# Performance work log

Measured on AMD Instinct MI355X. Metric: run time of the kernel, lower is better.

## Reference

```python
import jax, jax.numpy as jnp
import numpy as np

K_TOP = 2  # n_experts_per_tok
W_SCALE = 0.02  # keep activations numerically tame


def setup_inputs() -> dict:
    key = jax.random.key(0)
    ks = jax.random.split(key, 8)
    D, F, E = 1024, 1024, 8
    B, T = 4, 2048
    x = jax.random.normal(ks[0], (B, T, D), dtype=jnp.float32)
    router_w = jax.random.normal(ks[1], (D, E), dtype=jnp.float32) * W_SCALE
    sg = jax.random.normal(ks[2], (D, F), dtype=jnp.float32) * W_SCALE
    su = jax.random.normal(ks[3], (D, F), dtype=jnp.float32) * W_SCALE
    sd = jax.random.normal(ks[4], (F, D), dtype=jnp.float32) * W_SCALE
    wg = jax.random.normal(ks[5], (E, D, F), dtype=jnp.float32) * W_SCALE
    wu = jax.random.normal(ks[6], (E, D, F), dtype=jnp.float32) * W_SCALE
    wd = jax.random.normal(ks[7], (E, F, D), dtype=jnp.float32) * W_SCALE
    return {"x": x, "router_w": router_w, "sg": sg, "su": su, "sd": sd,
            "wg": wg, "wu": wu, "wd": wd}


def reference(x, router_w, sg, su, sd, wg, wu, wd):
    B, T, D = x.shape
    E = wg.shape[0]
    flat = x.reshape(-1, D)                       # [N, D]
    N = flat.shape[0]

    # shared SwiGLU expert (n_shared_experts = 1)
    shared = (jax.nn.silu(flat @ sg) * (flat @ su)) @ sd  # [N, D]

    # top-k softmax router with renormalization
    probs = jax.nn.softmax(flat @ router_w, axis=-1)      # [N, E]
    topk_p, topk_i = jax.lax.top_k(probs, K_TOP)          # [N, K]
    topk_p = topk_p / (jnp.sum(topk_p, axis=-1, keepdims=True) + 1e-9)

    # dense combine weights: scatter renormalized probs into [N, E]
    cw = jnp.zeros((N, E), dtype=flat.dtype).at[
        jnp.arange(N)[:, None], topk_i].add(topk_p)

    # per-expert SwiGLU on all tokens, weighted combine (jit-friendly MoE form)
    h = jax.nn.silu(jnp.einsum('nd,edf->nef', flat, wg)) \
        * jnp.einsum('nd,edf->nef', flat, wu)             # [N, E, F]
    eo = jnp.einsum('nef,efd->ned', h, wd)                # [N, E, D]
    routed = jnp.einsum('ned,ne->nd', eo, cw)             # [N, D]

    return (shared + routed).reshape(B, T, D)
```

## Files before the change

kernel.cpp:

```cpp
#include <hip/hip_runtime.h>

#define N_TOK    8192
#define D_DIM    1024
#define F_DIM    1024
#define NESH     9
#define MAX_RTD  17408
#define MAX_ROWS 26624
#define BT 128
#define BK 32
#define NK 32

#define MO 16
#define MT 25

typedef float  f4    __attribute__((ext_vector_type(4)));
typedef float  f32x4 __attribute__((ext_vector_type(4)));
typedef short  s16x8 __attribute__((ext_vector_type(8)));
typedef unsigned short u16x8 __attribute__((ext_vector_type(8)));
typedef unsigned short u16x4 __attribute__((ext_vector_type(4)));

static __device__ __forceinline__ unsigned short f2bf(float f) {
    union { float f; unsigned u; } v; v.f = f;
    unsigned r = v.u + 0x7FFFu + ((v.u >> 16) & 1u);
    return (unsigned short)(r >> 16);
}
static __device__ __forceinline__ float bf2f(unsigned short u) {
    union { unsigned u; float f; } v; v.u = ((unsigned)u) << 16; return v.f;
}

#define GLDS(gp, lp) __builtin_amdgcn_global_load_lds( \
    (const __attribute__((address_space(1))) void*)(gp), \
    (__attribute__((address_space(3))) void*)(lp), 16, 0, 0)

__global__ __launch_bounds__(256) void k_transpose(
    const float* __restrict__ wg, const float* __restrict__ wu,
    const float* __restrict__ wd, const float* __restrict__ sg,
    const float* __restrict__ su, const float* __restrict__ sd,
    unsigned short* __restrict__ wgt, unsigned short* __restrict__ wut,
    unsigned short* __restrict__ wdt)
{
    int bx = blockIdx.x;
    int m = bx >> 8;
    int tile = bx & 255;
    int ty = tile >> 4, tx = tile & 15;
    int set = m / 9, e = m % 9;
    const float* src; unsigned short* dst;
    if (set == 0)      { src = (e < 8) ? wg + (size_t)e*1048576 : sg; dst = wgt + (size_t)e*1048576; }
    else if (set == 1) { src = (e < 8) ? wu + (size_t)e*1048576 : su; dst = wut + (size_t)e*1048576; }
    else               { src = (e < 8) ? wd + (size_t)e*1048576 : sd; dst = wdt + (size_t)e*1048576; }

    __shared__ unsigned short ts[64 * 67];
    int t = threadIdx.x;
    int rT0 = ty * 64, cT0 = tx * 64;
    #pragma unroll
    for (int i = 0; i < 4; i++) {
        int idx = t + i * 256;
        int a  = idx >> 4;
        int b4 = (idx & 15) * 4;
        f4 v = *(const f4*)(src + (size_t)(cT0 + a) * 1024 + rT0 + b4);
        ts[a * 67 + b4 + 0] = f2bf(v[0]);
        ts[a * 67 + b4 + 1] = f2bf(v[1]);
        ts[a * 67 + b4 + 2] = f2bf(v[2]);
        ts[a * 67 + b4 + 3] = f2bf(v[3]);
    }
    __syncthreads();
    #pragma unroll
    for (int i = 0; i < 2; i++) {
        int slot = t + i * 256;
        int r  = slot >> 3;
        int c8 = (slot & 7) * 8;
        u16x8 o;
        #pragma unroll
        for (int k = 0; k < 8; k++) o[k] = ts[(c8 + k) * 67 + r];
        *(u16x8*)&dst[(size_t)(rT0 + r) * 1024 + cT0 + c8] = o;
    }
}

__global__ __launch_bounds__(256) void k_router(
    const float* __restrict__ x, const float* __restrict__ rw,
    unsigned short* __restrict__ xb,
    int* __restrict__ tk_i, float* __restrict__ tk_w)
{
    int wid = threadIdx.x >> 6, lane = threadIdx.x & 63;
    int n = blockIdx.x * 4 + wid;
    const float* xr = x + (size_t)n * D_DIM;
    unsigned short* xbr = xb + (size_t)n * D_DIM;
    float acc[8] = {0,0,0,0,0,0,0,0};
    #pragma unroll
    for (int it = 0; it < 4; it++) {
        int d0 = it * 256 + lane * 4;
        f4 xv = *(const f4*)(xr + d0);
        #pragma unroll
        for (int j = 0; j < 4; j++) {
            f4 r0 = *(const f4*)(rw + (size_t)(d0 + j) * 8);
            f4 r1 = *(const f4*)(rw + (size_t)(d0 + j) * 8 + 4);
            acc[0] += xv[j]*r0[0]; acc[1] += xv[j]*r0[1]; acc[2] += xv[j]*r0[2]; acc[3] += xv[j]*r0[3];
            acc[4] += xv[j]*r1[0]; acc[5] += xv[j]*r1[1]; acc[6] += xv[j]*r1[2]; acc[7] += xv[j]*r1[3];
        }
        u16x4 o; o[0]=f2bf(xv[0]); o[1]=f2bf(xv[1]); o[2]=f2bf(xv[2]); o[3]=f2bf(xv[3]);
        *(u16x4*)&xbr[d0] = o;
    }
    #pragma unroll
    for (int e = 0; e < 8; e++)
        for (int off = 32; off; off >>= 1)
            acc[e] += __shfl_xor(acc[e], off, 64);
    if (lane == 0) {
        float mx = acc[0];
        for (int e = 1; e < 8; e++) mx = fmaxf(mx, acc[e]);
        float p[8], s = 0.f;
        for (int e = 0; e < 8; e++) { p[e] = expf(acc[e] - mx); s += p[e]; }
        int i0 = 0;
        for (int e = 1; e < 8; e++) if (p[e] > p[i0]) i0 = e;
        int i1 = (i0 == 0) ? 1 : 0;
        for (int e = 0; e < 8; e++) if (e != i0 && p[e] > p[i1]) i1 = e;
        float p0 = p[i0] / s, p1 = p[i1] / s;
        float rs = p0 + p1 + 1e-9f;
        tk_i[2*n] = i0;  tk_i[2*n+1] = i1;
        tk_w[2*n] = p0 / rs;  tk_w[2*n+1] = p1 / rs;
    }
}

__global__ __launch_bounds__(1024) void k_count_scatter(
    const int* __restrict__ tk_i, const float* __restrict__ tk_w,
    int* __restrict__ meta,
    int* __restrict__ row_token, int* __restrict__ row_expert,
    int* __restrict__ tok_pos)
{
    __shared__ int cnt[1024 * 9];
    __shared__ int tot[8];
    __shared__ int off[9];
    const int t = threadIdx.x;
    const int lane = t & 63;
    const int wid = t >> 6;

    #pragma unroll
    for (int e = 0; e < 8; e++) cnt[t * 9 + e] = 0;
    __syncthreads();

    #pragma unroll
    for (int j = 0; j < 8; j++) {
        int n = t * 8 + j;
        cnt[t * 9 + tk_i[2 * n]]++;
        cnt[t * 9 + tk_i[2 * n + 1]]++;
    }
    __syncthreads();

    if (wid < 8) {
        const int e = wid;
        int carry = 0;
        for (int c = 0; c < 16; c++) {
            int i = c * 64 + lane;
            int v = cnt[i * 9 + e];
            int s = v;
            #pragma unroll
            for (int d = 1; d < 64; d <<= 1) {
                int u = __shfl_up(s, d, 64);
                if (lane >= d) s += u;
            }
            cnt[i * 9 + e] = s - v + carry;
            carry += __shfl(s, 63, 64);
        }
        if (lane == 0) tot[e] = carry;
    }
    __syncthreads();

    if (t == 0) {
        int acc = 0;
        #pragma unroll
        for (int e = 0; e < 8; e++) {
            off[e] = acc;
            meta[MO + e] = acc;
            acc += ((tot[e] + 127) >> 7) << 7;
        }
        off[8] = acc;
        meta[MO + 8] = acc;
        meta[MT] = acc + N_TOK;
    }
    __syncthreads();

    #pragma unroll
    for (int j = 0; j < 8; j++) {
        int n = t * 8 + j;
        #pragma unroll
        for (int k = 0; k < 2; k++) {
            int e = tk_i[2 * n + k];
            int pos = off[e] + cnt[t * 9 + e];
            cnt[t * 9 + e] = cnt[t * 9 + e] + 1;
            row_token[pos] = n; row_expert[pos] = e;
            tok_pos[2 * n + k] = pos;
        }
        int ps = off[8] + n;
        row_token[ps] = n; row_expert[ps] = 8;
    }
    #pragma unroll
    for (int e = 0; e < 8; e++) {
        int start = off[e] + tot[e], end = off[e + 1];
        for (int i = start + t; i < end; i += 1024) row_token[i] = -1;
    }
}


__global__ __launch_bounds__(512, 4) void k_gemm1(
    const unsigned short* __restrict__ xb,
    const unsigned short* __restrict__ wgt,
    const unsigned short* __restrict__ wut,
    const int* __restrict__ row_token,
    const int* __restrict__ row_expert,
    const int* __restrict__ meta,
    unsigned short* __restrict__ h)
{
    const int total = meta[MT];
    const int orig = blockIdx.x;
    const int bid = (orig & 7) * 208 + (orig >> 3);
    const int rt = bid >> 3, ct = bid & 7;
    const int row0 = rt * BT;
    if (row0 >= total) return;
    const int e = row_expert[row0];

    __shared__ __align__(16) unsigned short sA[2 * 128 * 32];
    __shared__ __align__(16) unsigned short sBg[2 * 128 * 32];
    __shared__ __align__(16) unsigned short sBu[2 * 128 * 32];

    const int t = threadIdx.x;
    const int lane = t & 63;
    const int lr = lane & 15;
    const int kl = lane >> 4;
    const int wid = t >> 6;
    const int wr = wid >> 2, wc = wid & 3;

    const int srow = t >> 2;
    const int scg  = (t & 3) ^ ((srow >> 1) & 3);
    int tok = row_token[row0 + srow];
    if (tok < 0) tok = 0;
    const unsigned short* srcA = xb + (size_t)tok * D_DIM + scg * 8;
    const unsigned short* srcG = wgt + ((size_t)e * F_DIM + ct * BT + srow) * D_DIM + scg * 8;
    const unsigned short* srcU = wut + ((size_t)e * F_DIM + ct * BT + srow) * D_DIM + scg * 8;

    f32x4 accg[4][2] = {}, accu[4][2] = {};

#define ST1(bb, k0) do { \
    GLDS(srcA + (k0), &sA[(bb) * 4096 + t * 8]); \
    GLDS(srcG + (k0), &sBg[(bb) * 4096 + t * 8]); \
    GLDS(srcU + (k0), &sBu[(bb) * 4096 + t * 8]); } while (0)

#define COMPUTE1(bb) do { \
    const unsigned short* pA  = &sA[(bb) * 4096]; \
    const unsigned short* pG  = &sBg[(bb) * 4096]; \
    const unsigned short* pU  = &sBu[(bb) * 4096]; \
    s16x8 a_[4], g_[2], q_[2]; \
    _Pragma("unroll") \
    for (int m_ = 0; m_ < 4; m_++) { \
        int row = wr * 64 + m_ * 16 + lr; \
        a_[m_] = *(const s16x8*)&pA[row * 32 + ((kl ^ ((row >> 1) & 3)) << 3)]; } \
    _Pragma("unroll") \
    for (int n_ = 0; n_ < 2; n_++) { \
        int row = wc * 32 + n_ * 16 + lr; \
        int ix = row * 32 + ((kl ^ ((row >> 1) & 3)) << 3); \
        g_[n_] = *(const s16x8*)&pG[ix]; \
        q_[n_] = *(const s16x8*)&pU[ix]; } \
    _Pragma("unroll") \
    for (int m_ = 0; m_ < 4; m_++) \
        _Pragma("unroll") \
        for (int n_ = 0; n_ < 2; n_++) { \
            accg[m_][n_] = __builtin_amdgcn_mfma_f32_16x16x32_bf16(a_[m_], g_[n_], accg[m_][n_], 0, 0, 0); \
            accu[m_][n_] = __builtin_amdgcn_mfma_f32_16x16x32_bf16(a_[m_], q_[n_], accu[m_][n_], 0, 0, 0); } \
    } while (0)

    ST1(0, 0);
    for (int u = 0; u < NK; u++) {
        if (u < NK - 1) {
            ST1((u + 1) & 1, (u + 1) * BK);
            asm volatile("s_waitcnt vmcnt(3)" ::: "memory");
        } else {
            asm volatile("s_waitcnt vmcnt(0)" ::: "memory");
        }
        __builtin_amdgcn_s_barrier();
        __builtin_amdgcn_s_setprio(1);
        COMPUTE1(u & 1);
        __builtin_amdgcn_s_setprio(0);
        asm volatile("" ::: "memory");
        __builtin_amdgcn_s_barrier();
    }

    #pragma unroll
    for (int m = 0; m < 4; m++)
        #pragma unroll
        for (int r = 0; r < 4; r++) {
            int grow = row0 + wr * 64 + m * 16 + (lane >> 4) * 4 + r;
            unsigned short* hrow = h + (size_t)grow * F_DIM + ct * BT + wc * 32 + lr;
            #pragma unroll
            for (int n = 0; n < 2; n++) {
                float g = accg[m][n][r], uu = accu[m][n][r];
                float sv = g / (1.f + __expf(-g));
                hrow[n * 16] = f2bf(sv * uu);
            }
        }
#undef ST1
#undef COMPUTE1
}

__global__ __launch_bounds__(512, 4) void k_gemm2(
    const unsigned short* __restrict__ h,
    const unsigned short* __restrict__ wdt,
    const int* __restrict__ row_expert,
    const int* __restrict__ meta,
    unsigned short* __restrict__ eo,
    float* __restrict__ out)
{
    const int total = meta[MT];
    const int off8 = meta[MO + 8];
    const int orig = blockIdx.x;
    const int bid = (orig & 7) * 208 + (orig >> 3);
    const int rt = bid >> 3, ct = bid & 7;
    const int row0 = rt * BT;
    if (row0 >= total) return;
    const int e = row_expert[row0];

    __shared__ __align__(16) unsigned short sA[2 * 128 * 32];
    __shared__ __align__(16) unsigned short sB[2 * 128 * 32];

    const int t = threadIdx.x;
    const int lane = t & 63;
    const int lr = lane & 15;
    const int kl = lane >> 4;
    const int wid = t >> 6;
    const int wr = wid >> 2, wc = wid & 3;

    const int srow = t >> 2;
    const int scg  = (t & 3) ^ ((srow >> 1) & 3);
    const unsigned short* srcA = h + (size_t)(row0 + srow) * F_DIM + scg * 8;
    const unsigned short* srcB = wdt + ((size_t)e * D_DIM + ct * BT + srow) * F_DIM + scg * 8;

    f32x4 acc[4][2] = {};

#define ST2(bb, k0) do { \
    GLDS(srcA + (k0), &sA[(bb) * 4096 + t * 8]); \
    GLDS(srcB + (k0), &sB[(bb) * 4096 + t * 8]); } while (0)

#define COMPUTE2(bb) do { \
    const unsigned short* pA = &sA[(bb) * 4096]; \
    const unsigned short* pB = &sB[(bb) * 4096]; \
    s16x8 a_[4], b_[2]; \
    _Pragma("unroll") \
    for (int m_ = 0; m_ < 4; m_++) { \
        int row = wr * 64 + m_ * 16 + lr; \
        a_[m_] = *(const s16x8*)&pA[row * 32 + ((kl ^ ((row >> 1) & 3)) << 3)]; } \
    _Pragma("unroll") \
    for (int n_ = 0; n_ < 2; n_++) { \
        int row = wc * 32 + n_ * 16 + lr; \
        b_[n_] = *(const s16x8*)&pB[row * 32 + ((kl ^ ((row >> 1) & 3)) << 3)]; } \
    _Pragma("unroll") \
    for (int m_ = 0; m_ < 4; m_++) \
        _Pragma("unroll") \
        for (int n_ = 0; n_ < 2; n_++) \
            acc[m_][n_] = __builtin_amdgcn_mfma_f32_16x16x32_bf16(a_[m_], b_[n_], acc[m_][n_], 0, 0, 0); \
    } while (0)

    ST2(0, 0);
    for (int u = 0; u < NK; u++) {
        if (u < NK - 1) {
            ST2((u + 1) & 1, (u + 1) * BK);
            asm volatile("s_waitcnt vmcnt(2)" ::: "memory");
        } else {
            asm volatile("s_waitcnt vmcnt(0)" ::: "memory");
        }
        __builtin_amdgcn_s_barrier();
        __builtin_amdgcn_s_setprio(1);
        COMPUTE2(u & 1);
        __builtin_amdgcn_s_setprio(0);
        asm volatile("" ::: "memory");
        __builtin_amdgcn_s_barrier();
    }

    if (e < 8) {
        #pragma unroll
        for (int m = 0; m < 4; m++)
            #pragma unroll
            for (int r = 0; r < 4; r++) {
                int grow = row0 + wr * 64 + m * 16 + (lane >> 4) * 4 + r;
                unsigned short* erow = eo + (size_t)grow * D_DIM + ct * BT + wc * 32 + lr;
                #pragma unroll
                for (int n = 0; n < 2; n++)
                    erow[n * 16] = f2bf(acc[m][n][r]);
            }
    } else {
        #pragma unroll
        for (int m = 0; m < 4; m++)
            #pragma unroll
            for (int r = 0; r < 4; r++) {
                int grow = row0 + wr * 64 + m * 16 + (lane >> 4) * 4 + r;
                int tok = grow - off8;
                float* orow = out + (size_t)tok * D_DIM + ct * BT + wc * 32 + lr;
                #pragma unroll
                for (int n = 0; n < 2; n++)
                    orow[n * 16] = acc[m][n][r];
            }
    }
#undef ST2
#undef COMPUTE2
}

__global__ __launch_bounds__(256) void k_combine(
    const unsigned short* __restrict__ eo,
    const int* __restrict__ tok_pos, const float* __restrict__ tk_w,
    float* __restrict__ out)
{
    const int t = threadIdx.x;
    const int n = blockIdx.x * 2 + (t >> 7);
    const int c0 = (t & 127) * 8;
    const int p0 = tok_pos[2 * n], p1 = tok_pos[2 * n + 1];
    const float w0 = tk_w[2 * n], w1 = tk_w[2 * n + 1];
    u16x8 a = *(const u16x8*)&eo[(size_t)p0 * D_DIM + c0];
    u16x8 b = *(const u16x8*)&eo[(size_t)p1 * D_DIM + c0];
    float* orow = out + (size_t)n * D_DIM + c0;
    f4 o0 = *(f4*)orow, o1 = *(f4*)(orow + 4);
    #pragma unroll
    for (int j = 0; j < 4; j++) {
        o0[j] += w0 * bf2f(a[j])     + w1 * bf2f(b[j]);
        o1[j] += w0 * bf2f(a[4 + j]) + w1 * bf2f(b[4 + j]);
    }
    *(f4*)orow = o0;
    *(f4*)(orow + 4) = o1;
}

extern "C" void kernel_launch(void* const* d_in, const int* in_sizes, int n_in,
                              void* d_out, int out_size, void* d_ws, size_t ws_size,
                              hipStream_t stream)
{
    const float* x  = (const float*)d_in[0];
    const float* rw = (const float*)d_in[1];
    const float* sg = (const float*)d_in[2];
    const float* su = (const float*)d_in[3];
    const float* sd = (const float*)d_in[4];
    const float* wg = (const float*)d_in[5];
    const float* wu = (const float*)d_in[6];
    const float* wd = (const float*)d_in[7];
    float* out = (float*)d_out;

    char* p = (char*)d_ws;
    unsigned short* xb  = (unsigned short*)p; p += (size_t)N_TOK * D_DIM * 2;
    unsigned short* wgt = (unsigned short*)p; p += (size_t)NESH * D_DIM * F_DIM * 2;
    unsigned short* wut = (unsigned short*)p; p += (size_t)NESH * D_DIM * F_DIM * 2;
    unsigned short* wdt = (unsigned short*)p; p += (size_t)NESH * D_DIM * F_DIM * 2;
    unsigned short* h   = (unsigned short*)p; p += (size_t)MAX_ROWS * F_DIM * 2;
    int*   row_token  = (int*)p;   p += (size_t)MAX_ROWS * 4;
    int*   row_expert = (int*)p;   p += (size_t)MAX_ROWS * 4;
    int*   tok_pos = (int*)p;      p += (size_t)N_TOK * 2 * 4;
    int*   tk_i = (int*)p;         p += (size_t)N_TOK * 2 * 4;
    float* tk_w = (float*)p;       p += (size_t)N_TOK * 2 * 4;
    int*   meta = (int*)p;         p += 1024;
    if ((size_t)(p - (char*)d_ws) > ws_size) return;

    unsigned short* eo = wgt;

    k_router<<<N_TOK / 4, 256, 0, stream>>>(x, rw, xb, tk_i, tk_w);
    k_transpose<<<27 * 256, 256, 0, stream>>>(wg, wu, wd, sg, su, sd, wgt, wut, wdt);
    k_count_scatter<<<1, 1024, 0, stream>>>(tk_i, tk_w, meta, row_token, row_expert, tok_pos);
    k_gemm1<<<(MAX_ROWS / BT) * 8, 512, 0, stream>>>(xb, wgt, wut, row_token, row_expert, meta, h);
    k_gemm2<<<(MAX_ROWS / BT) * 8, 512, 0, stream>>>(h, wdt, row_expert, meta, eo, out);
    k_combine<<<N_TOK / 2, 256, 0, stream>>>(eo, tok_pos, tk_w, out);
}
```

Before: 317.3 us.

## Enlarge down-projection GEMM tiles to 256x256 with BK=64 and 256-row padding

The second GEMM (h @ wd) moves from 128x128 output tiles with BK=32 to 256x256 tiles with BK=64. Each wave now accumulates an 8x4 grid of MFMA fragments, and LDS uses a 64-wide XOR swizzle. Expert segments are padded to 256 rows so a tile never spans two experts, and padding rows now get their expert id. The aim is more operand reuse per LDS load and fewer global loads. The cost is extra padded rows in both GEMMs, one large-LDS block per CU, higher register pressure and fewer blocks, which may cause wave-quantization imbalance.

```diff
diff --git a/kernel.cpp b/kernel.cpp
--- a/kernel.cpp
+++ b/kernel.cpp
@@ -4,11 +4,14 @@
 #define D_DIM    1024
 #define F_DIM    1024
 #define NESH     9
-#define MAX_RTD  17408
+#define MAX_RTD  18432
 #define MAX_ROWS 26624
 #define BT 128
 #define BK 32
 #define NK 32
+#define BM2 256
+#define BK2 64
+#define NK2 16
 
 #define MO 16
 #define MT 25
@@ -31,6 +34,8 @@
 #define GLDS(gp, lp) __builtin_amdgcn_global_load_lds( \
     (const __attribute__((address_space(1))) void*)(gp), \
     (__attribute__((address_space(3))) void*)(lp), 16, 0, 0)
+
+#define RSWZ64(row, idx) ((idx) ^ (((row) & 7) << 3))
 
 __global__ __launch_bounds__(256) void k_transpose(
     const float* __restrict__ wg, const float* __restrict__ wu,
@@ -170,7 +175,7 @@
         for (int e = 0; e < 8; e++) {
             off[e] = acc;
             meta[MO + e] = acc;
-            acc += ((tot[e] + 127) >> 7) << 7;
+            acc += ((tot[e] + 255) >> 8) << 8;
         }
         off[8] = acc;
         meta[MO + 8] = acc;
@@ -195,10 +200,12 @@
     #pragma unroll
     for (int e = 0; e < 8; e++) {
         int start = off[e] + tot[e], end = off[e + 1];
-        for (int i = start + t; i < end; i += 1024) row_token[i] = -1;
-    }
-}
-
+        for (int i = start + t; i < end; i += 1024) {
+            row_token[i] = -1;
+            row_expert[i] = e;
+        }
+    }
+}
 
 __global__ __launch_bounds__(512, 4) void k_gemm1(
     const unsigned short* __restrict__ xb,
@@ -299,7 +306,7 @@
 #undef COMPUTE1
 }
 
-__global__ __launch_bounds__(512, 4) void k_gemm2(
+__global__ __launch_bounds__(512, 2) void k_gemm2(
     const unsigned short* __restrict__ h,
     const unsigned short* __restrict__ wdt,
     const int* __restrict__ row_expert,
@@ -310,57 +317,74 @@
     const int total = meta[MT];
     const int off8 = meta[MO + 8];
     const int orig = blockIdx.x;
-    const int bid = (orig & 7) * 208 + (orig >> 3);
-    const int rt = bid >> 3, ct = bid & 7;
-    const int row0 = rt * BT;
+    const int bid = (orig & 7) * 52 + (orig >> 3);
+    const int rt = bid >> 2, ct = bid & 3;
+    const int row0 = rt * BM2;
     if (row0 >= total) return;
     const int e = row_expert[row0];
 
-    __shared__ __align__(16) unsigned short sA[2 * 128 * 32];
-    __shared__ __align__(16) unsigned short sB[2 * 128 * 32];
+    __shared__ __align__(16) unsigned short sA[2 * BM2 * BK2];
+    __shared__ __align__(16) unsigned short sB[2 * BM2 * BK2];
 
     const int t = threadIdx.x;
     const int lane = t & 63;
     const int lr = lane & 15;
-    const int kl = lane >> 4;
     const int wid = t >> 6;
     const int wr = wid >> 2, wc = wid & 3;
 
-    const int srow = t >> 2;
-    const int scg  = (t & 3) ^ ((srow >> 1) & 3);
-    const unsigned short* srcA = h + (size_t)(row0 + srow) * F_DIM + scg * 8;
-    const unsigned short* srcB = wdt + ((size_t)e * D_DIM + ct * BT + srow) * F_DIM + scg * 8;
-
-    f32x4 acc[4][2] = {};
-
-#define ST2(bb, k0) do { \
-    GLDS(srcA + (k0), &sA[(bb) * 4096 + t * 8]); \
-    GLDS(srcB + (k0), &sB[(bb) * 4096 + t * 8]); } while (0)
+    const unsigned short* asrc[4];
+    const unsigned short* bsrc[4];
+    #pragma unroll
+    for (int i = 0; i < 4; i++) {
+        int slot = t + i * 512;
+        int row = slot >> 3;
+        int cg  = (slot & 7) ^ (row & 7);
+        asrc[i] = h + (size_t)(row0 + row) * F_DIM + cg * 8;
+        bsrc[i] = wdt + ((size_t)e * D_DIM + ct * 256 + row) * F_DIM + cg * 8;
+    }
+
+    f32x4 acc[8][4] = {};
+
+#define STAGE_A2(bb, k0) do { \
+    unsigned short* dA = &sA[(bb) * (BM2 * BK2)]; \
+    _Pragma("unroll") \
+    for (int i_ = 0; i_ < 4; i_++) GLDS(asrc[i_] + (k0), &dA[(t + i_ * 512) * 8]); \
+    } while (0)
+#define STAGE_B2(bb, k0) do { \
+    unsigned short* dB = &sB[(bb) * (BM2 * BK2)]; \
+    _Pragma("unroll") \
+    for (int i_ = 0; i_ < 4; i_++) GLDS(bsrc[i_] + (k0), &dB[(t + i_ * 512) * 8]); \
+    } while (0)
 
 #define COMPUTE2(bb) do { \
-    const unsigned short* pA = &sA[(bb) * 4096]; \
-    const unsigned short* pB = &sB[(bb) * 4096]; \
-    s16x8 a_[4], b_[2]; \
-    _Pragma("unroll") \
-    for (int m_ = 0; m_ < 4; m_++) { \
-        int row = wr * 64 + m_ * 16 + lr; \
-        a_[m_] = *(const s16x8*)&pA[row * 32 + ((kl ^ ((row >> 1) & 3)) << 3)]; } \
-    _Pragma("unroll") \
-    for (int n_ = 0; n_ < 2; n_++) { \
-        int row = wc * 32 + n_ * 16 + lr; \
-        b_[n_] = *(const s16x8*)&pB[row * 32 + ((kl ^ ((row >> 1) & 3)) << 3)]; } \
-    _Pragma("unroll") \
-    for (int m_ = 0; m_ < 4; m_++) \
+    const unsigned short* pA = &sA[(bb) * (BM2 * BK2)]; \
+    const unsigned short* pB = &sB[(bb) * (BM2 * BK2)]; \
+    _Pragma("unroll") \
+    for (int kk = 0; kk < BK2; kk += 32) { \
+        const int koff = kk + (lane >> 4) * 8; \
+        s16x8 a_[8], b_[4]; \
         _Pragma("unroll") \
-        for (int n_ = 0; n_ < 2; n_++) \
-            acc[m_][n_] = __builtin_amdgcn_mfma_f32_16x16x32_bf16(a_[m_], b_[n_], acc[m_][n_], 0, 0, 0); \
-    } while (0)
-
-    ST2(0, 0);
-    for (int u = 0; u < NK; u++) {
-        if (u < NK - 1) {
-            ST2((u + 1) & 1, (u + 1) * BK);
-            asm volatile("s_waitcnt vmcnt(2)" ::: "memory");
+        for (int m_ = 0; m_ < 8; m_++) { \
+            int row = wr * 128 + m_ * 16 + lr; \
+            a_[m_] = *(const s16x8*)&pA[RSWZ64(row, row * BK2 + koff)]; } \
+        _Pragma("unroll") \
+        for (int n_ = 0; n_ < 4; n_++) { \
+            int row = wc * 64 + n_ * 16 + lr; \
+            b_[n_] = *(const s16x8*)&pB[RSWZ64(row, row * BK2 + koff)]; } \
+        _Pragma("unroll") \
+        for (int m_ = 0; m_ < 8; m_++) \
+            _Pragma("unroll") \
+            for (int n_ = 0; n_ < 4; n_++) \
+                acc[m_][n_] = __builtin_amdgcn_mfma_f32_16x16x32_bf16(a_[m_], b_[n_], acc[m_][n_], 0, 0, 0); \
+    } } while (0)
+
+    STAGE_A2(0, 0);
+    STAGE_B2(0, 0);
+    for (int u = 0; u < NK2; u++) {
+        if (u < NK2 - 1) {
+            STAGE_A2((u + 1) & 1, (u + 1) * BK2);
+            STAGE_B2((u + 1) & 1, (u + 1) * BK2);
+            asm volatile("s_waitcnt vmcnt(8)" ::: "memory");
         } else {
             asm volatile("s_waitcnt vmcnt(0)" ::: "memory");
         }
@@ -374,29 +398,30 @@
 
     if (e < 8) {
         #pragma unroll
-        for (int m = 0; m < 4; m++)
+        for (int mf = 0; mf < 8; mf++)
             #pragma unroll
             for (int r = 0; r < 4; r++) {
-                int grow = row0 + wr * 64 + m * 16 + (lane >> 4) * 4 + r;
-                unsigned short* erow = eo + (size_t)grow * D_DIM + ct * BT + wc * 32 + lr;
+                int grow = row0 + wr * 128 + mf * 16 + (lane >> 4) * 4 + r;
+                unsigned short* erow = eo + (size_t)grow * D_DIM + ct * 256 + wc * 64 + lr;
                 #pragma unroll
-                for (int n = 0; n < 2; n++)
-                    erow[n * 16] = f2bf(acc[m][n][r]);
+                for (int ni = 0; ni < 4; ni++)
+                    erow[ni * 16] = f2bf(acc[mf][ni][r]);
             }
     } else {
         #pragma unroll
-        for (int m = 0; m < 4; m++)
+        for (int mf = 0; mf < 8; mf++)
             #pragma unroll
             for (int r = 0; r < 4; r++) {
-                int grow = row0 + wr * 64 + m * 16 + (lane >> 4) * 4 + r;
+                int grow = row0 + wr * 128 + mf * 16 + (lane >> 4) * 4 + r;
                 int tok = grow - off8;
-                float* orow = out + (size_t)tok * D_DIM + ct * BT + wc * 32 + lr;
+                float* orow = out + (size_t)tok * D_DIM + ct * 256 + wc * 64 + lr;
                 #pragma unroll
-                for (int n = 0; n < 2; n++)
-                    orow[n * 16] = acc[m][n][r];
+                for (int ni = 0; ni < 4; ni++)
+                    orow[ni * 16] = acc[mf][ni][r];
             }
     }
-#undef ST2
+#undef STAGE_A2
+#undef STAGE_B2
 #undef COMPUTE2
 }
 
@@ -457,6 +482,6 @@
     k_transpose<<<27 * 256, 256, 0, stream>>>(wg, wu, wd, sg, su, sd, wgt, wut, wdt);
     k_count_scatter<<<1, 1024, 0, stream>>>(tk_i, tk_w, meta, row_token, row_expert, tok_pos);
     k_gemm1<<<(MAX_ROWS / BT) * 8, 512, 0, stream>>>(xb, wgt, wut, row_token, row_expert, meta, h);
-    k_gemm2<<<(MAX_ROWS / BT) * 8, 512, 0, stream>>>(h, wdt, row_expert, meta, eo, out);
+    k_gemm2<<<(MAX_ROWS / BM2) * 4, 512, 0, stream>>>(h, wdt, row_expert, meta, eo, out);
     k_combine<<<N_TOK / 2, 256, 0, stream>>>(eo, tok_pos, tk_w, out);
 }
```

Result: no change. 320.9 us (+1.1%).

## Enlarge MoE GEMM tiles to 256x256 with BK=64 and quadrant-interleaved pipeline

Applied to the files above, without the earlier changes.

Both grouped GEMMs move from 128x128 tiles with BK=32 to 256-row tiles with BK=64, computed as four 128x128 quadrants. Global-to-LDS loads of the next half-tiles are interleaved between quadrant MFMA phases. Expert row padding rises to multiples of 256, and padded rows now get an expert id. GEMM1 interleaves gate and up weight rows inside one B tile so one tile yields both. The aim is higher arithmetic intensity and less global traffic per FLOP, at the cost of 128 KB of LDS, lower occupancy (2 blocks per CU), more padding waste and more barriers.

```diff
diff --git a/kernel.cpp b/kernel.cpp
--- a/kernel.cpp
+++ b/kernel.cpp
@@ -4,11 +4,9 @@
 #define D_DIM    1024
 #define F_DIM    1024
 #define NESH     9
-#define MAX_RTD  17408
+#define MAX_RTD  18432
 #define MAX_ROWS 26624
-#define BT 128
-#define BK 32
-#define NK 32
+#define NKT 16
 
 #define MO 16
 #define MT 25
@@ -31,6 +29,10 @@
 #define GLDS(gp, lp) __builtin_amdgcn_global_load_lds( \
     (const __attribute__((address_space(1))) void*)(gp), \
     (__attribute__((address_space(3))) void*)(lp), 16, 0, 0)
+
+#define BARRIER __builtin_amdgcn_s_barrier()
+#define LGKM0 do { asm volatile("s_waitcnt lgkmcnt(0)" ::: "memory"); \
+                   __builtin_amdgcn_sched_barrier(0); } while (0)
 
 __global__ __launch_bounds__(256) void k_transpose(
     const float* __restrict__ wg, const float* __restrict__ wu,
@@ -170,7 +172,7 @@
         for (int e = 0; e < 8; e++) {
             off[e] = acc;
             meta[MO + e] = acc;
-            acc += ((tot[e] + 127) >> 7) << 7;
+            acc += ((tot[e] + 255) >> 8) << 8;
         }
         off[8] = acc;
         meta[MO + 8] = acc;
@@ -195,12 +197,14 @@
     #pragma unroll
     for (int e = 0; e < 8; e++) {
         int start = off[e] + tot[e], end = off[e + 1];
-        for (int i = start + t; i < end; i += 1024) row_token[i] = -1;
-    }
-}
-
-
-__global__ __launch_bounds__(512, 4) void k_gemm1(
+        for (int i = start + t; i < end; i += 1024) {
+            row_token[i] = -1;
+            row_expert[i] = e;
+        }
+    }
+}
+
+__global__ __launch_bounds__(512, 2) void k_gemm1(
     const unsigned short* __restrict__ xb,
     const unsigned short* __restrict__ wgt,
     const unsigned short* __restrict__ wut,
@@ -211,15 +215,14 @@
 {
     const int total = meta[MT];
     const int orig = blockIdx.x;
-    const int bid = (orig & 7) * 208 + (orig >> 3);
+    const int bid = (orig & 7) * 104 + (orig >> 3);
     const int rt = bid >> 3, ct = bid & 7;
-    const int row0 = rt * BT;
+    const int row0 = rt * 256;
     if (row0 >= total) return;
     const int e = row_expert[row0];
 
-    __shared__ __align__(16) unsigned short sA[2 * 128 * 32];
-    __shared__ __align__(16) unsigned short sBg[2 * 128 * 32];
-    __shared__ __align__(16) unsigned short sBu[2 * 128 * 32];
+    __shared__ __align__(16) unsigned short sA[4 * 128 * 64];
+    __shared__ __align__(16) unsigned short sB[4 * 128 * 64];
 
     const int t = threadIdx.x;
     const int lane = t & 63;
@@ -228,78 +231,112 @@
     const int wid = t >> 6;
     const int wr = wid >> 2, wc = wid & 3;
 
-    const int srow = t >> 2;
-    const int scg  = (t & 3) ^ ((srow >> 1) & 3);
-    int tok = row_token[row0 + srow];
-    if (tok < 0) tok = 0;
-    const unsigned short* srcA = xb + (size_t)tok * D_DIM + scg * 8;
-    const unsigned short* srcG = wgt + ((size_t)e * F_DIM + ct * BT + srow) * D_DIM + scg * 8;
-    const unsigned short* srcU = wut + ((size_t)e * F_DIM + ct * BT + srow) * D_DIM + scg * 8;
-
-    f32x4 accg[4][2] = {}, accu[4][2] = {};
-
-#define ST1(bb, k0) do { \
-    GLDS(srcA + (k0), &sA[(bb) * 4096 + t * 8]); \
-    GLDS(srcG + (k0), &sBg[(bb) * 4096 + t * 8]); \
-    GLDS(srcU + (k0), &sBu[(bb) * 4096 + t * 8]); } while (0)
-
-#define COMPUTE1(bb) do { \
-    const unsigned short* pA  = &sA[(bb) * 4096]; \
-    const unsigned short* pG  = &sBg[(bb) * 4096]; \
-    const unsigned short* pU  = &sBu[(bb) * 4096]; \
-    s16x8 a_[4], g_[2], q_[2]; \
-    _Pragma("unroll") \
-    for (int m_ = 0; m_ < 4; m_++) { \
-        int row = wr * 64 + m_ * 16 + lr; \
-        a_[m_] = *(const s16x8*)&pA[row * 32 + ((kl ^ ((row >> 1) & 3)) << 3)]; } \
-    _Pragma("unroll") \
-    for (int n_ = 0; n_ < 2; n_++) { \
-        int row = wc * 32 + n_ * 16 + lr; \
-        int ix = row * 32 + ((kl ^ ((row >> 1) & 3)) << 3); \
-        g_[n_] = *(const s16x8*)&pG[ix]; \
-        q_[n_] = *(const s16x8*)&pU[ix]; } \
-    _Pragma("unroll") \
-    for (int m_ = 0; m_ < 4; m_++) \
-        _Pragma("unroll") \
-        for (int n_ = 0; n_ < 2; n_++) { \
-            accg[m_][n_] = __builtin_amdgcn_mfma_f32_16x16x32_bf16(a_[m_], g_[n_], accg[m_][n_], 0, 0, 0); \
-            accu[m_][n_] = __builtin_amdgcn_mfma_f32_16x16x32_bf16(a_[m_], q_[n_], accu[m_][n_], 0, 0, 0); } \
-    } while (0)
-
-    ST1(0, 0);
-    for (int u = 0; u < NK; u++) {
-        if (u < NK - 1) {
-            ST1((u + 1) & 1, (u + 1) * BK);
-            asm volatile("s_waitcnt vmcnt(3)" ::: "memory");
+    const unsigned short* apt[2][2];
+    const unsigned short* bpt[2][2];
+    #pragma unroll
+    for (int hh = 0; hh < 2; hh++)
+        #pragma unroll
+        for (int s2 = 0; s2 < 2; s2++) {
+            int slot = t + s2 * 512;
+            int rl = slot >> 3;
+            int ch = (slot & 7) ^ (rl & 7);
+            int r = hh * 128 + rl;
+            int tok = row_token[row0 + r];
+            if (tok < 0) tok = 0;
+            apt[hh][s2] = xb + (size_t)tok * D_DIM + ch * 8;
+            int mat = (r >> 4) & 1;
+            int f = ct * 128 + (r & 15) + ((r >> 5) << 4);
+            bpt[hh][s2] = (mat ? wut : wgt) + ((size_t)e * F_DIM + f) * D_DIM + ch * 8;
+        }
+
+#define LDS_A1(b, hh) (&sA[(((b) << 1) | (hh)) * 8192])
+#define LDS_B1(b, hh) (&sB[(((b) << 1) | (hh)) * 8192])
+#define STG_A1(kt, hh) do { int _b = (kt) & 1; \
+    GLDS(apt[hh][0] + (kt) * 64, LDS_A1(_b, hh) + t * 8); \
+    GLDS(apt[hh][1] + (kt) * 64, LDS_A1(_b, hh) + (t + 512) * 8); } while (0)
+#define STG_B1(kt, hh) do { int _b = (kt) & 1; \
+    GLDS(bpt[hh][0] + (kt) * 64, LDS_B1(_b, hh) + t * 8); \
+    GLDS(bpt[hh][1] + (kt) * 64, LDS_B1(_b, hh) + (t + 512) * 8); } while (0)
+
+    s16x8 aF[4][2], bF[2][2];
+    f32x4 acc[2][2][4][2] = {};
+
+#define RD_A1(b, mh) do { const unsigned short* p = LDS_A1(b, mh); \
+    _Pragma("unroll") for (int m_ = 0; m_ < 4; m_++) { \
+        int r1 = wr * 64 + m_ * 16 + lr; \
+        int base = r1 * 64, sw = (r1 & 7) << 3; \
+        aF[m_][0] = *(const s16x8*)&p[(base + kl * 8) ^ sw]; \
+        aF[m_][1] = *(const s16x8*)&p[(base + 32 + kl * 8) ^ sw]; } } while (0)
+#define RD_B1(b, nh) do { const unsigned short* p = LDS_B1(b, nh); \
+    _Pragma("unroll") for (int n_ = 0; n_ < 2; n_++) { \
+        int r1 = wc * 32 + n_ * 16 + lr; \
+        int base = r1 * 64, sw = (r1 & 7) << 3; \
+        bF[n_][0] = *(const s16x8*)&p[(base + kl * 8) ^ sw]; \
+        bF[n_][1] = *(const s16x8*)&p[(base + 32 + kl * 8) ^ sw]; } } while (0)
+#define QMM1(mh, nh) do { \
+    _Pragma("unroll") for (int m_ = 0; m_ < 4; m_++) \
+    _Pragma("unroll") for (int n_ = 0; n_ < 2; n_++) { \
+        acc[mh][nh][m_][n_] = __builtin_amdgcn_mfma_f32_16x16x32_bf16(aF[m_][0], bF[n_][0], acc[mh][nh][m_][n_], 0, 0, 0); \
+        acc[mh][nh][m_][n_] = __builtin_amdgcn_mfma_f32_16x16x32_bf16(aF[m_][1], bF[n_][1], acc[mh][nh][m_][n_], 0, 0, 0); } } while (0)
+
+    STG_A1(0, 0); STG_B1(0, 0); STG_A1(0, 1); STG_B1(0, 1);
+    STG_A1(1, 0); STG_B1(1, 1);
+    asm volatile("s_waitcnt vmcnt(4)" ::: "memory");
+    BARRIER;
+
+    for (int kt = 0; kt < NKT; kt++) {
+        const int b = kt & 1;
+        RD_A1(b, 0); RD_B1(b, 0);
+        if (kt + 1 < NKT) STG_A1(kt + 1, 1);
+        BARRIER; LGKM0;
+        __builtin_amdgcn_s_setprio(1); QMM1(0, 0); __builtin_amdgcn_s_setprio(0);
+        BARRIER;
+        RD_B1(b, 1);
+        if (kt + 1 < NKT) STG_B1(kt + 1, 0);
+        BARRIER; LGKM0;
+        __builtin_amdgcn_s_setprio(1); QMM1(0, 1); __builtin_amdgcn_s_setprio(0);
+        BARRIER;
+        RD_A1(b, 1);
+        if (kt + 2 < NKT) STG_A1(kt + 2, 0);
+        BARRIER; LGKM0;
+        __builtin_amdgcn_s_setprio(1); QMM1(1, 1); __builtin_amdgcn_s_setprio(0);
+        BARRIER;
+        RD_B1(b, 0);
+        if (kt + 2 < NKT) {
+            STG_B1(kt + 2, 1);
+            asm volatile("s_waitcnt vmcnt(4)" ::: "memory");
         } else {
             asm volatile("s_waitcnt vmcnt(0)" ::: "memory");
         }
-        __builtin_amdgcn_s_barrier();
-        __builtin_amdgcn_s_setprio(1);
-        COMPUTE1(u & 1);
-        __builtin_amdgcn_s_setprio(0);
-        asm volatile("" ::: "memory");
-        __builtin_amdgcn_s_barrier();
-    }
-
-    #pragma unroll
-    for (int m = 0; m < 4; m++)
-        #pragma unroll
-        for (int r = 0; r < 4; r++) {
-            int grow = row0 + wr * 64 + m * 16 + (lane >> 4) * 4 + r;
-            unsigned short* hrow = h + (size_t)grow * F_DIM + ct * BT + wc * 32 + lr;
+        BARRIER; LGKM0;
+        __builtin_amdgcn_s_setprio(1); QMM1(1, 0); __builtin_amdgcn_s_setprio(0);
+        BARRIER;
+    }
+
+    #pragma unroll
+    for (int mh = 0; mh < 2; mh++)
+        #pragma unroll
+        for (int nh = 0; nh < 2; nh++)
             #pragma unroll
-            for (int n = 0; n < 2; n++) {
-                float g = accg[m][n][r], uu = accu[m][n][r];
-                float sv = g / (1.f + __expf(-g));
-                hrow[n * 16] = f2bf(sv * uu);
-            }
-        }
-#undef ST1
-#undef COMPUTE1
-}
-
-__global__ __launch_bounds__(512, 4) void k_gemm2(
+            for (int m = 0; m < 4; m++)
+                #pragma unroll
+                for (int r = 0; r < 4; r++) {
+                    int row = row0 + mh * 128 + wr * 64 + m * 16 + (lane >> 4) * 4 + r;
+                    int f = ct * 128 + nh * 64 + wc * 16 + lr;
+                    float g = acc[mh][nh][m][0][r], uu = acc[mh][nh][m][1][r];
+                    float sv = g / (1.f + __expf(-g));
+                    h[(size_t)row * F_DIM + f] = f2bf(sv * uu);
+                }
+#undef LDS_A1
+#undef LDS_B1
+#undef STG_A1
+#undef STG_B1
+#undef RD_A1
+#undef RD_B1
+#undef QMM1
+}
+
+__global__ __launch_bounds__(512, 2) void k_gemm2(
     const unsigned short* __restrict__ h,
     const unsigned short* __restrict__ wdt,
     const int* __restrict__ row_expert,
@@ -310,14 +347,14 @@
     const int total = meta[MT];
     const int off8 = meta[MO + 8];
     const int orig = blockIdx.x;
-    const int bid = (orig & 7) * 208 + (orig >> 3);
-    const int rt = bid >> 3, ct = bid & 7;
-    const int row0 = rt * BT;
+    const int bid = (orig & 7) * 52 + (orig >> 3);
+    const int rt = bid >> 2, ct = bid & 3;
+    const int row0 = rt * 256;
     if (row0 >= total) return;
     const int e = row_expert[row0];
 
-    __shared__ __align__(16) unsigned short sA[2 * 128 * 32];
-    __shared__ __align__(16) unsigned short sB[2 * 128 * 32];
+    __shared__ __align__(16) unsigned short sA[4 * 128 * 64];
+    __shared__ __align__(16) unsigned short sB[4 * 128 * 64];
 
     const int t = threadIdx.x;
     const int lane = t & 63;
@@ -326,78 +363,121 @@
     const int wid = t >> 6;
     const int wr = wid >> 2, wc = wid & 3;
 
-    const int srow = t >> 2;
-    const int scg  = (t & 3) ^ ((srow >> 1) & 3);
-    const unsigned short* srcA = h + (size_t)(row0 + srow) * F_DIM + scg * 8;
-    const unsigned short* srcB = wdt + ((size_t)e * D_DIM + ct * BT + srow) * F_DIM + scg * 8;
-
-    f32x4 acc[4][2] = {};
-
-#define ST2(bb, k0) do { \
-    GLDS(srcA + (k0), &sA[(bb) * 4096 + t * 8]); \
-    GLDS(srcB + (k0), &sB[(bb) * 4096 + t * 8]); } while (0)
-
-#define COMPUTE2(bb) do { \
-    const unsigned short* pA = &sA[(bb) * 4096]; \
-    const unsigned short* pB = &sB[(bb) * 4096]; \
-    s16x8 a_[4], b_[2]; \
-    _Pragma("unroll") \
-    for (int m_ = 0; m_ < 4; m_++) { \
-        int row = wr * 64 + m_ * 16 + lr; \
-        a_[m_] = *(const s16x8*)&pA[row * 32 + ((kl ^ ((row >> 1) & 3)) << 3)]; } \
-    _Pragma("unroll") \
-    for (int n_ = 0; n_ < 2; n_++) { \
-        int row = wc * 32 + n_ * 16 + lr; \
-        b_[n_] = *(const s16x8*)&pB[row * 32 + ((kl ^ ((row >> 1) & 3)) << 3)]; } \
-    _Pragma("unroll") \
-    for (int m_ = 0; m_ < 4; m_++) \
-        _Pragma("unroll") \
-        for (int n_ = 0; n_ < 2; n_++) \
-            acc[m_][n_] = __builtin_amdgcn_mfma_f32_16x16x32_bf16(a_[m_], b_[n_], acc[m_][n_], 0, 0, 0); \
-    } while (0)
-
-    ST2(0, 0);
-    for (int u = 0; u < NK; u++) {
-        if (u < NK - 1) {
-            ST2((u + 1) & 1, (u + 1) * BK);
-            asm volatile("s_waitcnt vmcnt(2)" ::: "memory");
+    const unsigned short* apt[2][2];
+    const unsigned short* bpt[2][2];
+    #pragma unroll
+    for (int hh = 0; hh < 2; hh++)
+        #pragma unroll
+        for (int s2 = 0; s2 < 2; s2++) {
+            int slot = t + s2 * 512;
+            int rl = slot >> 3;
+            int ch = (slot & 7) ^ (rl & 7);
+            int r = hh * 128 + rl;
+            apt[hh][s2] = h + (size_t)(row0 + r) * F_DIM + ch * 8;
+            bpt[hh][s2] = wdt + ((size_t)e * D_DIM + ct * 256 + r) * F_DIM + ch * 8;
+        }
+
+#define LDS_A2(b, hh) (&sA[(((b) << 1) | (hh)) * 8192])
+#define LDS_B2(b, hh) (&sB[(((b) << 1) | (hh)) * 8192])
+#define STG_A2(kt, hh) do { int _b = (kt) & 1; \
+    GLDS(apt[hh][0] + (kt) * 64, LDS_A2(_b, hh) + t * 8); \
+    GLDS(apt[hh][1] + (kt) * 64, LDS_A2(_b, hh) + (t + 512) * 8); } while (0)
+#define STG_B2(kt, hh) do { int _b = (kt) & 1; \
+    GLDS(bpt[hh][0] + (kt) * 64, LDS_B2(_b, hh) + t * 8); \
+    GLDS(bpt[hh][1] + (kt) * 64, LDS_B2(_b, hh) + (t + 512) * 8); } while (0)
+
+    s16x8 aF[4][2], bF[2][2];
+    f32x4 acc[2][2][4][2] = {};
+
+#define RD_A2(b, mh) do { const unsigned short* p = LDS_A2(b, mh); \
+    _Pragma("unroll") for (int m_ = 0; m_ < 4; m_++) { \
+        int r1 = wr * 64 + m_ * 16 + lr; \
+        int base = r1 * 64, sw = (r1 & 7) << 3; \
+        aF[m_][0] = *(const s16x8*)&p[(base + kl * 8) ^ sw]; \
+        aF[m_][1] = *(const s16x8*)&p[(base + 32 + kl * 8) ^ sw]; } } while (0)
+#define RD_B2(b, nh) do { const unsigned short* p = LDS_B2(b, nh); \
+    _Pragma("unroll") for (int n_ = 0; n_ < 2; n_++) { \
+        int r1 = wc * 32 + n_ * 16 + lr; \
+        int base = r1 * 64, sw = (r1 & 7) << 3; \
+        bF[n_][0] = *(const s16x8*)&p[(base + kl * 8) ^ sw]; \
+        bF[n_][1] = *(const s16x8*)&p[(base + 32 + kl * 8) ^ sw]; } } while (0)
+#define QMM2(mh, nh) do { \
+    _Pragma("unroll") for (int m_ = 0; m_ < 4; m_++) \
+    _Pragma("unroll") for (int n_ = 0; n_ < 2; n_++) { \
+        acc[mh][nh][m_][n_] = __builtin_amdgcn_mfma_f32_16x16x32_bf16(aF[m_][0], bF[n_][0], acc[mh][nh][m_][n_], 0, 0, 0); \
+        acc[mh][nh][m_][n_] = __builtin_amdgcn_mfma_f32_16x16x32_bf16(aF[m_][1], bF[n_][1], acc[mh][nh][m_][n_], 0, 0, 0); } } while (0)
+
+    STG_A2(0, 0); STG_B2(0, 0); STG_A2(0, 1); STG_B2(0, 1);
+    STG_A2(1, 0); STG_B2(1, 1);
+    asm volatile("s_waitcnt vmcnt(4)" ::: "memory");
+    BARRIER;
+
+    for (int kt = 0; kt < NKT; kt++) {
+        const int b = kt & 1;
+        RD_A2(b, 0); RD_B2(b, 0);
+        if (kt + 1 < NKT) STG_A2(kt + 1, 1);
+        BARRIER; LGKM0;
+        __builtin_amdgcn_s_setprio(1); QMM2(0, 0); __builtin_amdgcn_s_setprio(0);
+        BARRIER;
+        RD_B2(b, 1);
+        if (kt + 1 < NKT) STG_B2(kt + 1, 0);
+        BARRIER; LGKM0;
+        __builtin_amdgcn_s_setprio(1); QMM2(0, 1); __builtin_amdgcn_s_setprio(0);
+        BARRIER;
+        RD_A2(b, 1);
+        if (kt + 2 < NKT) STG_A2(kt + 2, 0);
+        BARRIER; LGKM0;
+        __builtin_amdgcn_s_setprio(1); QMM2(1, 1); __builtin_amdgcn_s_setprio(0);
+        BARRIER;
+        RD_B2(b, 0);
+        if (kt + 2 < NKT) {
+            STG_B2(kt + 2, 1);
+            asm volatile("s_waitcnt vmcnt(4)" ::: "memory");
         } else {
             asm volatile("s_waitcnt vmcnt(0)" ::: "memory");
         }
-        __builtin_amdgcn_s_barrier();
-        __builtin_amdgcn_s_setprio(1);
-        COMPUTE2(u & 1);
-        __builtin_amdgcn_s_setprio(0);
-        asm volatile("" ::: "memory");
-        __builtin_amdgcn_s_barrier();
+        BARRIER; LGKM0;
+        __builtin_amdgcn_s_setprio(1); QMM2(1, 0); __builtin_amdgcn_s_setprio(0);
+        BARRIER;
     }
 
     if (e < 8) {
         #pragma unroll
-        for (int m = 0; m < 4; m++)
+        for (int mh = 0; mh < 2; mh++)
             #pragma unroll
-            for (int r = 0; r < 4; r++) {
-                int grow = row0 + wr * 64 + m * 16 + (lane >> 4) * 4 + r;
-                unsigned short* erow = eo + (size_t)grow * D_DIM + ct * BT + wc * 32 + lr;
+            for (int nh = 0; nh < 2; nh++)
                 #pragma unroll
-                for (int n = 0; n < 2; n++)
-                    erow[n * 16] = f2bf(acc[m][n][r]);
-            }
+                for (int m = 0; m < 4; m++)
+                    #pragma unroll
+                    for (int r = 0; r < 4; r++) {
+                        int row = row0 + mh * 128 + wr * 64 + m * 16 + (lane >> 4) * 4 + r;
+                        unsigned short* erow = eo + (size_t)row * D_DIM + ct * 256 + nh * 128 + wc * 32 + lr;
+                        erow[0]  = f2bf(acc[mh][nh][m][0][r]);
+                        erow[16] = f2bf(acc[mh][nh][m][1][r]);
+                    }
     } else {
         #pragma unroll
-        for (int m = 0; m < 4; m++)
+        for (int mh = 0; mh < 2; mh++)
             #pragma unroll
-            for (int r = 0; r < 4; r++) {
-                int grow = row0 + wr * 64 + m * 16 + (lane >> 4) * 4 + r;
-                int tok = grow - off8;
-                float* orow = out + (size_t)tok * D_DIM + ct * BT + wc * 32 + lr;
+            for (int nh = 0; nh < 2; nh++)
                 #pragma unroll
-                for (int n = 0; n < 2; n++)
-                    orow[n * 16] = acc[m][n][r];
-            }
-    }
-#undef ST2
-#undef COMPUTE2
+                for (int m = 0; m < 4; m++)
+                    #pragma unroll
+                    for (int r = 0; r < 4; r++) {
+                        int row = row0 + mh * 128 + wr * 64 + m * 16 + (lane >> 4) * 4 + r;
+                        int tok = row - off8;
+                        float* orow = out + (size_t)tok * D_DIM + ct * 256 + nh * 128 + wc * 32 + lr;
+                        orow[0]  = acc[mh][nh][m][0][r];
+                        orow[16] = acc[mh][nh][m][1][r];
+                    }
+    }
+#undef LDS_A2
+#undef LDS_B2
+#undef STG_A2
+#undef STG_B2
+#undef RD_A2
+#undef RD_B2
+#undef QMM2
 }
 
 __global__ __launch_bounds__(256) void k_combine(
@@ -456,7 +536,7 @@
     k_router<<<N_TOK / 4, 256, 0, stream>>>(x, rw, xb, tk_i, tk_w);
     k_transpose<<<27 * 256, 256, 0, stream>>>(wg, wu, wd, sg, su, sd, wgt, wut, wdt);
     k_count_scatter<<<1, 1024, 0, stream>>>(tk_i, tk_w, meta, row_token, row_expert, tok_pos);
-    k_gemm1<<<(MAX_ROWS / BT) * 8, 512, 0, stream>>>(xb, wgt, wut, row_token, row_expert, meta, h);
-    k_gemm2<<<(MAX_ROWS / BT) * 8, 512, 0, stream>>>(h, wdt, row_expert, meta, eo, out);
+    k_gemm1<<<(MAX_ROWS / 256) * 8, 512, 0, stream>>>(xb, wgt, wut, row_token, row_expert, meta, h);
+    k_gemm2<<<(MAX_ROWS / 256) * 4, 512, 0, stream>>>(h, wdt, row_expert, meta, eo, out);
     k_combine<<<N_TOK / 2, 256, 0, stream>>>(eo, tok_pos, tk_w, out);
 }
```

Measured after the change: 326.9 us. 3.0% more time.
